# Performance work log

Measured on AMD Instinct MI355X. Metric: run time of the kernel, lower is better.

The kernel has to match this reference:

```python
import jax, jax.numpy as jnp
import numpy as np

D_MODEL = 1024
NUM_HEADS = 16
D_K = D_MODEL // NUM_HEADS
NEG = -10000.0


def setup_inputs() -> dict:
    key = jax.random.key(0)
    ks = jax.random.split(key, 8)
    B, S = 2, 2048
    query = jax.random.normal(ks[0], (B, S, D_MODEL), dtype=jnp.float32)
    key_t = jax.random.normal(ks[1], (B, S, D_MODEL), dtype=jnp.float32)
    value = jax.random.normal(ks[2], (B, S, D_MODEL), dtype=jnp.float32)
    mask = jax.random.randint(ks[3], (B, S), 0, 2, dtype=jnp.int32)
    scale = 1.0 / np.sqrt(D_MODEL)
    Wq = jax.random.normal(ks[4], (D_MODEL, D_MODEL), dtype=jnp.float32) * scale
    Wk = jax.random.normal(ks[5], (D_MODEL, D_MODEL), dtype=jnp.float32) * scale
    Wv = jax.random.normal(ks[6], (D_MODEL, D_MODEL), dtype=jnp.float32) * scale
    Wo = jax.random.normal(ks[7], (D_MODEL, D_MODEL), dtype=jnp.float32) * scale
    return {"query": query, "key": key_t, "value": value, "mask": mask,
            "Wq": Wq, "Wk": Wk, "Wv": Wv, "Wo": Wo}


def reference(query, key, value, mask, Wq, Wk, Wv, Wo):
    B, Sq, _ = query.shape
    Sk = key.shape[1]
    # Linear projections (torch Linear: x @ W.T), split heads -> [B,H,S,d_k]
    def proj(x, W, S):
        return (x @ W.T).reshape(B, S, NUM_HEADS, D_K).transpose(0, 2, 1, 3)
    Q = proj(query, Wq, Sq)
    K = proj(key, Wk, Sk)
    V = proj(value, Wv, Sk)
    # scores [B,H,Sq,Sk]
    scores = jnp.einsum("bhqd,bhkd->bhqk", Q, K) / jnp.sqrt(jnp.float32(D_K))
    # padding mask [B,Sk] -> [B,1,1,Sk]
    pad = mask[:, None, None, :]
    scores = jnp.where(pad == 0, NEG, scores)
    # causal mask (mask_future=True)
    causal = jnp.tril(jnp.ones((Sq, Sk), dtype=bool))
    scores = jnp.where(causal, scores, NEG)
    probs = jax.nn.softmax(scores, axis=-1)  # dropout p=0.0 -> identity
    out = jnp.einsum("bhqk,bhkd->bhqd", probs, V)
    out = out.transpose(0, 2, 1, 3).reshape(B, Sq, D_MODEL)
    return out @ Wo.T
```

## Files before the change

### kernel.cpp

```cpp
#include <hip/hip_runtime.h>
#include <hip/hip_bf16.h>
#include <math.h>

typedef __attribute__((ext_vector_type(8))) short s16x8;
typedef __attribute__((ext_vector_type(4))) float f32x4;

#define MFMA16(a,b,c) __builtin_amdgcn_mfma_f32_16x16x32_bf16((a),(b),(c),0,0,0)

#define GLD16(gp, lp) __builtin_amdgcn_global_load_lds( \
  (const __attribute__((address_space(1))) unsigned int*)(gp), \
  (__attribute__((address_space(3))) unsigned int*)(lp), 16, 0, 0)

static __device__ __forceinline__ unsigned short f2bu(float f) {
  __hip_bfloat16 h = __float2bfloat16(f);
  unsigned short u; __builtin_memcpy(&u, &h, 2); return u;
}
static __device__ __forceinline__ float b2f(unsigned short u) {
  unsigned int x = ((unsigned int)u) << 16; float f; __builtin_memcpy(&f, &x, 4); return f;
}

__global__ __launch_bounds__(256) void cast_all(const float* __restrict__ q, const float* __restrict__ k,
                                                const float* __restrict__ v,
                                                const float* __restrict__ Wq, const float* __restrict__ Wk,
                                                const float* __restrict__ Wv, const float* __restrict__ Wo,
                                                unsigned short* __restrict__ qc, unsigned short* __restrict__ kc,
                                                unsigned short* __restrict__ vc,
                                                unsigned short* __restrict__ wq, unsigned short* __restrict__ wk,
                                                unsigned short* __restrict__ wv, unsigned short* __restrict__ wo) {
  const int y = blockIdx.y;
  const float* in; unsigned short* out; int n4;
  switch (y) {
    case 0: in = q;  out = qc; n4 = 1048576; break;
    case 1: in = k;  out = kc; n4 = 1048576; break;
    case 2: in = v;  out = vc; n4 = 1048576; break;
    case 3: in = Wq; out = wq; n4 = 262144; break;
    case 4: in = Wk; out = wk; n4 = 262144; break;
    case 5: in = Wv; out = wv; n4 = 262144; break;
    default: in = Wo; out = wo; n4 = 262144; break;
  }
  int i = blockIdx.x * 256 + threadIdx.x;
  if (i < n4) {
    float4 val = *(const float4*)(in + (size_t)i * 4);
    unsigned int p0 = (unsigned int)f2bu(val.x) | ((unsigned int)f2bu(val.y) << 16);
    unsigned int p1 = (unsigned int)f2bu(val.z) | ((unsigned int)f2bu(val.w) << 16);
    uint2 pk; pk.x = p0; pk.y = p1;
    *(uint2*)(out + (size_t)i * 4) = pk;
  }
}

static __device__ __forceinline__ void gemm_core(const unsigned short* __restrict__ Aw,
                                                 const unsigned short* __restrict__ Bw,
                                                 int m0, int n0,
                                                 f32x4 (&acc)[4][4],
                                                 unsigned short (*As)[64], unsigned short (*Bs)[64]) {
  const int K = 1024;
  const int tid = threadIdx.x;
  const int lane = tid & 63, wave = tid >> 6;
  const int wm = wave >> 1, wn = wave & 1;
  const int row16 = lane & 15, kgrp = lane >> 4;
  const int srow = lane >> 3, sslot = (lane & 7) ^ srow;
  const int sw = row16 & 7;

  for (int k0 = 0; k0 < K; k0 += 64) {
#pragma unroll
    for (int i = 0; i < 4; i++) {
      int rr = (wave * 4 + i) * 8 + srow;
      GLD16(Aw + (size_t)(m0 + rr) * K + k0 + sslot * 8, (char*)As + (wave * 4 + i) * 1024);
      GLD16(Bw + (size_t)(n0 + rr) * K + k0 + sslot * 8, (char*)Bs + (wave * 4 + i) * 1024);
    }
    __syncthreads();

#pragma unroll
    for (int kk = 0; kk < 2; kk++) {
      s16x8 af[4], bfr[4];
#pragma unroll
      for (int mi = 0; mi < 4; mi++) {
        int rr = wm * 64 + mi * 16 + row16;
        af[mi] = *(const s16x8*)((char*)&As[rr][0] + ((kk * 4 + kgrp) ^ sw) * 16);
      }
#pragma unroll
      for (int ni = 0; ni < 4; ni++) {
        int rr = wn * 64 + ni * 16 + row16;
        bfr[ni] = *(const s16x8*)((char*)&Bs[rr][0] + ((kk * 4 + kgrp) ^ sw) * 16);
      }
#pragma unroll
      for (int mi = 0; mi < 4; mi++)
#pragma unroll
        for (int ni = 0; ni < 4; ni++)
          acc[mi][ni] = MFMA16(af[mi], bfr[ni], acc[mi][ni]);
    }
    __syncthreads();
  }
}

__global__ __launch_bounds__(256) void qkv_gemm(const unsigned short* __restrict__ qc,
                                                const unsigned short* __restrict__ kc,
                                                const unsigned short* __restrict__ vc,
                                                const unsigned short* __restrict__ Wqb,
                                                const unsigned short* __restrict__ Wkb,
                                                const unsigned short* __restrict__ Wvb,
                                                unsigned short* __restrict__ Qb,
                                                unsigned short* __restrict__ Kb,
                                                unsigned short* __restrict__ Vt) {
  __shared__ unsigned short As[128][64];
  __shared__ unsigned short Bs[128][64];
  const int xcd = blockIdx.x & 7, u = blockIdx.x >> 3;
  const int g = xcd * 12 + (u >> 3);
  const int z = g >> 5, mstrip = g & 31;
  const int m0 = mstrip * 128, n0 = (u & 7) * 128;

  const unsigned short* A = (z == 0) ? qc : (z == 1) ? kc : vc;
  const unsigned short* Bw = (z == 0) ? Wqb : (z == 1) ? Wkb : Wvb;

  f32x4 acc[4][4] = {};
  gemm_core(A, Bw, m0, n0, acc, As, Bs);

  const int lane = threadIdx.x & 63, wave = threadIdx.x >> 6;
  const int wm = wave >> 1, wn = wave & 1;
  const int row16 = lane & 15, kgrp = lane >> 4;

  if (z < 2) {
    unsigned short* C = z ? Kb : Qb;
#pragma unroll
    for (int mi = 0; mi < 4; mi++)
#pragma unroll
      for (int ni = 0; ni < 4; ni++)
#pragma unroll
        for (int r = 0; r < 4; r++) {
          int row = m0 + wm * 64 + mi * 16 + kgrp * 4 + r;
          int col = n0 + wn * 64 + ni * 16 + row16;
          C[(size_t)row * 1024 + col] = f2bu(acc[mi][ni][r]);
        }
  } else {
#pragma unroll
    for (int mi = 0; mi < 4; mi++)
#pragma unroll
      for (int ni = 0; ni < 4; ni++) {
        int mb = m0 + wm * 64 + mi * 16 + kgrp * 4;
        int col = n0 + wn * 64 + ni * 16 + row16;
        int bb = mb >> 11, s = mb & 2047;
        unsigned int p0 = (unsigned int)f2bu(acc[mi][ni][0]) | ((unsigned int)f2bu(acc[mi][ni][1]) << 16);
        unsigned int p1 = (unsigned int)f2bu(acc[mi][ni][2]) | ((unsigned int)f2bu(acc[mi][ni][3]) << 16);
        uint2 pk; pk.x = p0; pk.y = p1;
        *(uint2*)&Vt[(((size_t)(bb * 1024 + col)) << 11) + s] = pk;
      }
  }
}

__global__ __launch_bounds__(256) void gemm_wo(const unsigned short* __restrict__ A,
                                               const unsigned short* __restrict__ Bw,
                                               float* __restrict__ C) {
  __shared__ unsigned short As[128][64];
  __shared__ unsigned short Bs[128][64];
  const int xcd = blockIdx.x & 7, u = blockIdx.x >> 3;
  const int g = xcd * 4 + (u >> 3);
  const int m0 = g * 128, n0 = (u & 7) * 128;

  f32x4 acc[4][4] = {};
  gemm_core(A, Bw, m0, n0, acc, As, Bs);

  const int lane = threadIdx.x & 63, wave = threadIdx.x >> 6;
  const int wm = wave >> 1, wn = wave & 1;
  const int row16 = lane & 15, kgrp = lane >> 4;
#pragma unroll
  for (int mi = 0; mi < 4; mi++)
#pragma unroll
    for (int ni = 0; ni < 4; ni++)
#pragma unroll
      for (int r = 0; r < 4; r++) {
        int row = m0 + wm * 64 + mi * 16 + kgrp * 4 + r;
        int col = n0 + wn * 64 + ni * 16 + row16;
        C[(size_t)row * 1024 + col] = acc[mi][ni][r];
      }
}

__global__ __launch_bounds__(256) void fu_pen_kernel(const int* __restrict__ mask, int* __restrict__ fu,
                                                     float* __restrict__ pen) {
  const int S = 2048;
  int b = blockIdx.x;
  __shared__ int red[256];
  int best = S;
  for (int k = threadIdx.x; k < S; k += 256) {
    int mv = mask[b * S + k];
    pen[b * S + k] = mv ? 0.0f : -30000.0f;
    if (mv != 0 && k < best) best = k;
  }
  red[threadIdx.x] = best;
  __syncthreads();
  for (int s = 128; s > 0; s >>= 1) {
    if (threadIdx.x < s) red[threadIdx.x] = min(red[threadIdx.x], red[threadIdx.x + s]);
    __syncthreads();
  }
  if (threadIdx.x == 0) fu[b] = red[0];
}

__global__ __launch_bounds__(256) void reduce_vt(const unsigned short* __restrict__ Vt,
                                                 float* __restrict__ vsum) {
  __shared__ float red[256];
  const unsigned short* p = Vt + ((size_t)blockIdx.x << 11) + threadIdx.x * 8;
  uint4 u = *(const uint4*)p;
  float s = b2f((unsigned short)(u.x & 0xffff));
  s += b2f((unsigned short)(u.x >> 16));
  s += b2f((unsigned short)(u.y & 0xffff));
  s += b2f((unsigned short)(u.y >> 16));
  s += b2f((unsigned short)(u.z & 0xffff));
  s += b2f((unsigned short)(u.z >> 16));
  s += b2f((unsigned short)(u.w & 0xffff));
  s += b2f((unsigned short)(u.w >> 16));
  red[threadIdx.x] = s;
  __syncthreads();
  for (int st = 128; st > 0; st >>= 1) {
    if (threadIdx.x < st) red[threadIdx.x] += red[threadIdx.x + st];
    __syncthreads();
  }
  if (threadIdx.x == 0) vsum[blockIdx.x] = red[0];
}

__global__ __launch_bounds__(256) void flash_attn5(const unsigned short* __restrict__ Q,
                                                   const unsigned short* __restrict__ Kp,
                                                   const unsigned short* __restrict__ Vt,
                                                   const float* __restrict__ pen,
                                                   const int* __restrict__ fu,
                                                   const float* __restrict__ vsum,
                                                   unsigned short* __restrict__ O) {
  const int S = 2048, DM = 1024;
  const float SCALE2 = 0.125f * 1.4426950408889634f;
  const int bid = blockIdx.x;
  const int qt = 31 - (bid >> 5);
  const int bh = bid & 31;
  const int b = bh >> 4, h = bh & 15;
  const int tid = threadIdx.x, lane = tid & 63, wave = tid >> 6;
  const int row16 = lane & 15, kgrp = lane >> 4;

  __shared__ unsigned short Ks[2][64][64];
  __shared__ unsigned short Vs[2][64][64];
  __shared__ unsigned short Ps[4][16][72];

  const size_t base = ((size_t)b * S) * DM + h * 64;
  const size_t vtb = ((size_t)(b * 1024 + h * 64)) * S;
  const float* penb = pen + b * S;

  const int srow = lane >> 3;
  const int sslot = (lane & 7) ^ srow;
  const int sw = row16 & 7;

  const int q0 = qt * 64 + wave * 16;
  const int qg = q0 + row16;
  const int nt = qt + 1;

  s16x8 qf0 = *(const s16x8*)&Q[base + (size_t)qg * DM + kgrp * 8];
  s16x8 qf1 = *(const s16x8*)&Q[base + (size_t)qg * DM + 32 + kgrp * 8];

  f32x4 oacc[4] = {};
  float m_run = -1e30f, l_run = 0.f;

  auto stage = [&](int t, int bf) {
    const int kb = t * 64;
#pragma unroll
    for (int c2 = 0; c2 < 2; c2++) {
      const int r = wave * 16 + c2 * 8 + srow;
      GLD16(Kp + base + (size_t)(kb + r) * DM + sslot * 8,
            (char*)&Ks[bf][0][0] + (wave * 2 + c2) * 1024);
      GLD16(Vt + vtb + (size_t)r * S + kb + sslot * 8,
            (char*)&Vs[bf][0][0] + (wave * 2 + c2) * 1024);
    }
  };

  stage(0, 0);
  asm volatile("s_waitcnt vmcnt(0)" ::: "memory");
  __syncthreads();

  int cur = 0;
  for (int t = 0; t < nt; ++t) {
    if (t + 1 < nt) stage(t + 1, cur ^ 1);
    const int kb = t * 64;

    float4 pv[4];
#pragma unroll
    for (int nf = 0; nf < 4; nf++)
      pv[nf] = *(const float4*)&penb[kb + nf * 16 + kgrp * 4];

    f32x4 sc[4];
#pragma unroll
    for (int nf = 0; nf < 4; nf++) {
      const int rr = nf * 16 + row16;
      s16x8 k0 = *(const s16x8*)&Ks[cur][rr][(kgrp ^ sw) * 8];
      s16x8 k1 = *(const s16x8*)&Ks[cur][rr][((4 + kgrp) ^ sw) * 8];
      f32x4 a = {};
      a = MFMA16(k0, qf0, a);
      a = MFMA16(k1, qf1, a);
      sc[nf] = a;
    }

#pragma unroll
    for (int nf = 0; nf < 4; nf++) {
      sc[nf][0] = fmaf(sc[nf][0], SCALE2, pv[nf].x);
      sc[nf][1] = fmaf(sc[nf][1], SCALE2, pv[nf].y);
      sc[nf][2] = fmaf(sc[nf][2], SCALE2, pv[nf].z);
      sc[nf][3] = fmaf(sc[nf][3], SCALE2, pv[nf].w);
    }
    if (t == nt - 1) {
#pragma unroll
      for (int nf = 0; nf < 4; nf++) {
        const int kbase = kb + nf * 16 + kgrp * 4;
#pragma unroll
        for (int r = 0; r < 4; r++)
          if (kbase + r > qg) sc[nf][r] = -30000.0f;
      }
    }

    float t01 = fmaxf(fmaxf(sc[0][0], sc[0][1]), fmaxf(sc[0][2], sc[0][3]));
    float t23 = fmaxf(fmaxf(sc[1][0], sc[1][1]), fmaxf(sc[1][2], sc[1][3]));
    float t45 = fmaxf(fmaxf(sc[2][0], sc[2][1]), fmaxf(sc[2][2], sc[2][3]));
    float t67 = fmaxf(fmaxf(sc[3][0], sc[3][1]), fmaxf(sc[3][2], sc[3][3]));
    float tmax = fmaxf(fmaxf(t01, t23), fmaxf(t45, t67));
    tmax = fmaxf(tmax, __shfl_xor(tmax, 16));
    tmax = fmaxf(tmax, __shfl_xor(tmax, 32));

    if (__any(tmax > m_run)) {
      float mnew = fmaxf(m_run, tmax);
      float alpha = __builtin_exp2f(m_run - mnew);
      m_run = mnew;
      l_run *= alpha;
#pragma unroll
      for (int nf2 = 0; nf2 < 4; nf2++)
#pragma unroll
        for (int r = 0; r < 4; r++) oacc[nf2][r] *= alpha;
    }

    float rsum = 0.f;
#pragma unroll
    for (int nf = 0; nf < 4; nf++)
#pragma unroll
      for (int r = 0; r < 4; r++) {
        float p = __builtin_exp2f(sc[nf][r] - m_run);
        sc[nf][r] = p;
        rsum += p;
      }
    rsum += __shfl_xor(rsum, 16);
    rsum += __shfl_xor(rsum, 32);
    l_run += rsum;

#pragma unroll
    for (int nf = 0; nf < 4; nf++) {
      uint2 pk;
      pk.x = (unsigned int)f2bu(sc[nf][0]) | ((unsigned int)f2bu(sc[nf][1]) << 16);
      pk.y = (unsigned int)f2bu(sc[nf][2]) | ((unsigned int)f2bu(sc[nf][3]) << 16);
      *(uint2*)&Ps[wave][row16][nf * 16 + kgrp * 4] = pk;
    }
    s16x8 pf0 = *(const s16x8*)&Ps[wave][row16][kgrp * 8];
    s16x8 pf1 = *(const s16x8*)&Ps[wave][row16][32 + kgrp * 8];

#pragma unroll
    for (int nf2 = 0; nf2 < 4; nf2++) {
      const int rr = nf2 * 16 + row16;
      s16x8 v0 = *(const s16x8*)&Vs[cur][rr][(kgrp ^ sw) * 8];
      s16x8 v1 = *(const s16x8*)&Vs[cur][rr][((4 + kgrp) ^ sw) * 8];
      oacc[nf2] = MFMA16(v0, pf0, oacc[nf2]);
      oacc[nf2] = MFMA16(v1, pf1, oacc[nf2]);
    }

    asm volatile("s_waitcnt vmcnt(0)" ::: "memory");
    __syncthreads();
    cur ^= 1;
  }

  const int fub = fu[b];
  const float* vs = vsum + b * DM + h * 64;
  const float rl = 1.0f / l_run;
#pragma unroll
  for (int nf2 = 0; nf2 < 4; nf2++) {
    const int d0 = nf2 * 16 + kgrp * 4;
    float v0 = oacc[nf2][0] * rl, v1 = oacc[nf2][1] * rl;
    float v2 = oacc[nf2][2] * rl, v3 = oacc[nf2][3] * rl;
    if (qg < fub) {
      float4 vv = *(const float4*)&vs[d0];
      v0 = vv.x * (1.0f / 2048.0f);
      v1 = vv.y * (1.0f / 2048.0f);
      v2 = vv.z * (1.0f / 2048.0f);
      v3 = vv.w * (1.0f / 2048.0f);
    }
    uint2 pk;
    pk.x = (unsigned int)f2bu(v0) | ((unsigned int)f2bu(v1) << 16);
    pk.y = (unsigned int)f2bu(v2) | ((unsigned int)f2bu(v3) << 16);
    *(uint2*)&O[base + (size_t)qg * DM + d0] = pk;
  }
}

extern "C" void kernel_launch(void* const* d_in, const int* in_sizes, int n_in,
                              void* d_out, int out_size, void* d_ws, size_t ws_size,
                              hipStream_t stream) {
  const float* q    = (const float*)d_in[0];
  const float* k    = (const float*)d_in[1];
  const float* v    = (const float*)d_in[2];
  const int*   mask = (const int*)d_in[3];
  const float* Wq   = (const float*)d_in[4];
  const float* Wk   = (const float*)d_in[5];
  const float* Wv   = (const float*)d_in[6];
  const float* Wo   = (const float*)d_in[7];
  float* out = (float*)d_out;
  char* ws = (char*)d_ws;

  unsigned short* Wqb  = (unsigned short*)(ws + (size_t)0);
  unsigned short* Wkb  = (unsigned short*)(ws + ((size_t)2 << 20));
  unsigned short* Wvb  = (unsigned short*)(ws + ((size_t)4 << 20));
  unsigned short* Wob  = (unsigned short*)(ws + ((size_t)6 << 20));
  unsigned short* vc   = (unsigned short*)(ws + ((size_t)8 << 20));
  unsigned short* attn = (unsigned short*)(ws + ((size_t)8 << 20));
  unsigned short* Qb   = (unsigned short*)(ws + ((size_t)16 << 20));
  unsigned short* Kb   = (unsigned short*)(ws + ((size_t)24 << 20));
  unsigned short* Vt   = (unsigned short*)(ws + ((size_t)32 << 20));
  float* vsum          = (float*)(ws + ((size_t)40 << 20));
  int*   fub           = (int*)(ws + ((size_t)40 << 20) + (64 << 10));
  float* pen           = (float*)(ws + ((size_t)40 << 20) + (68 << 10));
  unsigned short* qc   = (unsigned short*)d_out;
  unsigned short* kc   = (unsigned short*)d_out + 4194304;

  cast_all<<<dim3(4096, 7), 256, 0, stream>>>(q, k, v, Wq, Wk, Wv, Wo,
                                              qc, kc, vc, Wqb, Wkb, Wvb, Wob);

  qkv_gemm<<<768, 256, 0, stream>>>(qc, kc, vc, Wqb, Wkb, Wvb, Qb, Kb, Vt);

  fu_pen_kernel<<<2, 256, 0, stream>>>(mask, fub, pen);
  reduce_vt<<<2048, 256, 0, stream>>>(Vt, vsum);

  flash_attn5<<<1024, 256, 0, stream>>>(Qb, Kb, Vt, pen, fub, vsum, attn);

  gemm_wo<<<256, 256, 0, stream>>>(attn, Wob, out);
}
```

Measured before the change: 144.8 us.

## Compute softmax row sums via MFMA with ones, swizzle P buffer, add setprio

Replaces the per-lane exp sum and cross-lane shuffle reductions with an MFMA that multiplies a ones vector by the bf16 P fragments, accumulating the row sums in an MFMA accumulator. The P shared buffer drops its padding and uses an XOR swizzle to avoid bank conflicts. s_setprio hints are added around the MFMA sections to favour matrix issue across waves. The sum now uses bf16-rounded probabilities, which slightly changes the numerics but matches the values that multiply V.

```diff
diff --git a/kernel.cpp b/kernel.cpp
--- a/kernel.cpp
+++ b/kernel.cpp
@@ -216,7 +216,7 @@
   if (threadIdx.x == 0) vsum[blockIdx.x] = red[0];
 }
 
-__global__ __launch_bounds__(256) void flash_attn5(const unsigned short* __restrict__ Q,
+__global__ __launch_bounds__(256) void flash_attn6(const unsigned short* __restrict__ Q,
                                                    const unsigned short* __restrict__ Kp,
                                                    const unsigned short* __restrict__ Vt,
                                                    const float* __restrict__ pen,
@@ -234,7 +234,7 @@
 
   __shared__ unsigned short Ks[2][64][64];
   __shared__ unsigned short Vs[2][64][64];
-  __shared__ unsigned short Ps[4][16][72];
+  __shared__ unsigned short Ps[4][16][64];
 
   const size_t base = ((size_t)b * S) * DM + h * 64;
   const size_t vtb = ((size_t)(b * 1024 + h * 64)) * S;
@@ -251,8 +251,12 @@
   s16x8 qf0 = *(const s16x8*)&Q[base + (size_t)qg * DM + kgrp * 8];
   s16x8 qf1 = *(const s16x8*)&Q[base + (size_t)qg * DM + 32 + kgrp * 8];
 
+  const short ONE = 0x3F80;
+  const s16x8 ones8 = {ONE, ONE, ONE, ONE, ONE, ONE, ONE, ONE};
+
   f32x4 oacc[4] = {};
-  float m_run = -1e30f, l_run = 0.f;
+  f32x4 lacc = {};
+  float m_run = -1e30f;
 
   auto stage = [&](int t, int bf) {
     const int kb = t * 64;
@@ -281,6 +285,7 @@
       pv[nf] = *(const float4*)&penb[kb + nf * 16 + kgrp * 4];
 
     f32x4 sc[4];
+    __builtin_amdgcn_s_setprio(1);
 #pragma unroll
     for (int nf = 0; nf < 4; nf++) {
       const int rr = nf * 16 + row16;
@@ -291,6 +296,7 @@
       a = MFMA16(k1, qf1, a);
       sc[nf] = a;
     }
+    __builtin_amdgcn_s_setprio(0);
 
 #pragma unroll
     for (int nf = 0; nf < 4; nf++) {
@@ -321,36 +327,33 @@
       float mnew = fmaxf(m_run, tmax);
       float alpha = __builtin_exp2f(m_run - mnew);
       m_run = mnew;
-      l_run *= alpha;
+      lacc[0] *= alpha; lacc[1] *= alpha; lacc[2] *= alpha; lacc[3] *= alpha;
 #pragma unroll
       for (int nf2 = 0; nf2 < 4; nf2++)
 #pragma unroll
         for (int r = 0; r < 4; r++) oacc[nf2][r] *= alpha;
     }
 
-    float rsum = 0.f;
 #pragma unroll
     for (int nf = 0; nf < 4; nf++)
 #pragma unroll
-      for (int r = 0; r < 4; r++) {
-        float p = __builtin_exp2f(sc[nf][r] - m_run);
-        sc[nf][r] = p;
-        rsum += p;
-      }
-    rsum += __shfl_xor(rsum, 16);
-    rsum += __shfl_xor(rsum, 32);
-    l_run += rsum;
+      for (int r = 0; r < 4; r++)
+        sc[nf][r] = __builtin_exp2f(sc[nf][r] - m_run);
 
 #pragma unroll
     for (int nf = 0; nf < 4; nf++) {
       uint2 pk;
       pk.x = (unsigned int)f2bu(sc[nf][0]) | ((unsigned int)f2bu(sc[nf][1]) << 16);
       pk.y = (unsigned int)f2bu(sc[nf][2]) | ((unsigned int)f2bu(sc[nf][3]) << 16);
-      *(uint2*)&Ps[wave][row16][nf * 16 + kgrp * 4] = pk;
-    }
-    s16x8 pf0 = *(const s16x8*)&Ps[wave][row16][kgrp * 8];
-    s16x8 pf1 = *(const s16x8*)&Ps[wave][row16][32 + kgrp * 8];
-
+      const int slot = (nf * 2 + (kgrp >> 1)) ^ sw;
+      *(uint2*)((char*)&Ps[wave][row16][0] + slot * 16 + (kgrp & 1) * 8) = pk;
+    }
+    s16x8 pf0 = *(const s16x8*)((char*)&Ps[wave][row16][0] + (kgrp ^ sw) * 16);
+    s16x8 pf1 = *(const s16x8*)((char*)&Ps[wave][row16][0] + ((4 + kgrp) ^ sw) * 16);
+
+    __builtin_amdgcn_s_setprio(1);
+    lacc = MFMA16(ones8, pf0, lacc);
+    lacc = MFMA16(ones8, pf1, lacc);
 #pragma unroll
     for (int nf2 = 0; nf2 < 4; nf2++) {
       const int rr = nf2 * 16 + row16;
@@ -359,6 +362,7 @@
       oacc[nf2] = MFMA16(v0, pf0, oacc[nf2]);
       oacc[nf2] = MFMA16(v1, pf1, oacc[nf2]);
     }
+    __builtin_amdgcn_s_setprio(0);
 
     asm volatile("s_waitcnt vmcnt(0)" ::: "memory");
     __syncthreads();
@@ -367,7 +371,7 @@
 
   const int fub = fu[b];
   const float* vs = vsum + b * DM + h * 64;
-  const float rl = 1.0f / l_run;
+  const float rl = 1.0f / lacc[0];
 #pragma unroll
   for (int nf2 = 0; nf2 < 4; nf2++) {
     const int d0 = nf2 * 16 + kgrp * 4;
@@ -424,7 +428,7 @@
   fu_pen_kernel<<<2, 256, 0, stream>>>(mask, fub, pen);
   reduce_vt<<<2048, 256, 0, stream>>>(Vt, vsum);
 
-  flash_attn5<<<1024, 256, 0, stream>>>(Qb, Kb, Vt, pen, fub, vsum, attn);
+  flash_attn6<<<1024, 256, 0, stream>>>(Qb, Kb, Vt, pen, fub, vsum, attn);
 
   gemm_wo<<<256, 256, 0, stream>>>(attn, Wob, out);
 }
```

New measurement: 143.3 us. No clear change (-1.0%).
